# Performance work log

Hardware: AMD Instinct MI355X
Metric: run time of the kernel (lower is better)

## Reference

```python
import jax, jax.numpy as jnp
import numpy as np
from jax import lax

B = 16384
NWIRES = 4


def _conv(x, w, b):
    # NCHW conv, stride 1, SAME padding (pad 1 for k=3)
    y = lax.conv_general_dilated(x, w, (1, 1), ((1, 1), (1, 1)),
                                 dimension_numbers=("NCHW", "OIHW", "NCHW"))
    return y + b[None, :, None, None]


def _pool2(x):
    b, c, h, w = x.shape
    return x.reshape(b, c, h // 2, 2, w // 2, 2).max(axis=(3, 5))


def _apply_1q(state, U, wire):
    # state: (B,2,2,2,2) complex; U: (B,2,2) complex
    s = jnp.moveaxis(state, wire + 1, -1)
    s = jnp.einsum("bij,b...j->b...i", U, s)
    return jnp.moveaxis(s, -1, wire + 1)


def _apply_cnot(state, c, t):
    s0 = jnp.take(state, 0, axis=c + 1)
    s1 = jnp.take(state, 1, axis=c + 1)
    ta = t + 1 if t < c else t  # target axis index after removing control axis
    s1 = jnp.flip(s1, axis=ta)
    return jnp.stack([s0, s1], axis=c + 1)


def _ry(th):
    c = jnp.cos(th / 2)
    s = jnp.sin(th / 2)
    U = jnp.stack([jnp.stack([c, -s], -1), jnp.stack([s, c], -1)], -2)
    return U.astype(jnp.complex64)


def _rz(th):
    e = jnp.exp(-0.5j * th.astype(jnp.complex64))
    z = jnp.zeros_like(e)
    return jnp.stack([jnp.stack([e, z], -1), jnp.stack([z, jnp.conj(e)], -1)], -2)


def _rx(th):
    c = jnp.cos(th / 2).astype(jnp.complex64)
    s = jnp.sin(th / 2).astype(jnp.complex64)
    return jnp.stack([jnp.stack([c, -1j * s], -1), jnp.stack([-1j * s, c], -1)], -2)


def _circuit(params):
    # params: (B, 16) -> PauliZ expvals (B, 4)
    b = params.shape[0]
    state = jnp.zeros((b, 16), jnp.complex64).at[:, 0].set(1.0).reshape(b, 2, 2, 2, 2)
    for i in range(NWIRES):
        state = _apply_1q(state, _ry(params[:, 4 * i + 0]), i)
        state = _apply_1q(state, _rz(params[:, 4 * i + 1]), i)
        state = _apply_1q(state, _rx(params[:, 4 * i + 2]), i)
        state = _apply_cnot(state, i, (i + 1) % NWIRES)
    probs = state.real ** 2 + state.imag ** 2  # (B,2,2,2,2)
    zs = []
    for i in range(NWIRES):
        p = probs.sum(axis=tuple(a for a in range(1, 5) if a != i + 1))  # (B,2)
        zs.append(p[:, 0] - p[:, 1])
    return jnp.stack(zs, axis=-1)


def setup_inputs() -> dict:
    key = jax.random.key(0)
    ks = jax.random.split(key, 12)
    d = {}
    d["x"] = jax.random.normal(ks[0], (B, 1, 28, 28), jnp.float32)
    d["conv1_w"] = jax.random.normal(ks[1], (4, 1, 3, 3), jnp.float32) * 0.3
    d["conv1_b"] = jax.random.normal(ks[2], (4,), jnp.float32) * 0.1
    d["conv2_w"] = jax.random.normal(ks[3], (4, 4, 3, 3), jnp.float32) * 0.15
    d["conv2_b"] = jax.random.normal(ks[4], (4,), jnp.float32) * 0.1
    d["pl_w"] = jax.random.normal(ks[5], (16, 196), jnp.float32) * 0.07
    d["pl_b"] = jax.random.normal(ks[6], (16,), jnp.float32) * 0.05
    d["ro_w"] = jax.random.normal(ks[7], (4, 4), jnp.float32) * 0.5
    d["ro_b"] = jax.random.normal(ks[8], (4,), jnp.float32) * 0.1
    d["bn_w"] = jnp.ones((4,), jnp.float32)
    d["bn_b"] = jnp.zeros((4,), jnp.float32)
    return d


def reference(x, conv1_w, conv1_b, conv2_w, conv2_b, pl_w, pl_b, ro_w, ro_b, bn_w, bn_b):
    h = _pool2(jax.nn.relu(_conv(x, conv1_w, conv1_b)))   # (B,4,14,14)
    h = _pool2(jax.nn.relu(_conv(h, conv2_w, conv2_b)))   # (B,4,7,7)
    flat = h.reshape(x.shape[0], -1)                      # (B,196)
    params = flat @ pl_w.T + pl_b                         # (B,16)
    z = _circuit(params)                                  # (B,4)
    out = z @ ro_w.T + ro_b                               # (B,4)
    mean = out.mean(0)
    var = out.var(0)  # biased, matches torch BN training normalization
    return (out - mean) / jnp.sqrt(var + 1e-5) * bn_w + bn_b
```

## Files before the change

### kernel.cpp

```cpp
#include <hip/hip_runtime.h>
#include <math.h>

#define BATCH 16384

typedef float v2f __attribute__((ext_vector_type(2)));

__device__ __forceinline__ v2f pk_fma(v2f a, v2f b, v2f c) {
  return __builtin_elementwise_fma(a, b, c);
}
__device__ __forceinline__ v2f pk_max(v2f a, v2f b) {
  return __builtin_elementwise_max(a, b);
}

__device__ __forceinline__ unsigned bf2(float lo, float hi) {
  unsigned a = __float_as_uint(lo);
  unsigned b = __float_as_uint(hi);
  a = (a + 0x7fffu + ((a >> 16) & 1u)) >> 16;
  b = (b + 0x7fffu + ((b >> 16) & 1u)) & 0xffff0000u;
  return a | b;
}

__global__ __launch_bounds__(256) void qnat_fused(
    const float* __restrict__ x,
    const float* __restrict__ w1,
    const float* __restrict__ b1,
    const float* __restrict__ w2,
    const float* __restrict__ b2,
    const float* __restrict__ plw,
    const float* __restrict__ plb,
    const float* __restrict__ rw,
    const float* __restrict__ rb,
    float* __restrict__ pre,
    float* __restrict__ stats)
{
  __shared__ __align__(16) float h1p[4][4 * 288 + 16];
  __shared__ __align__(16) float h2[4][4][200];
  __shared__ __align__(16) uint4 plw_tb[25 * 16];
  __shared__ float s_red[4][8];

  const int tid = threadIdx.x;
  const int w = tid >> 6;
  const int lane = tid & 63;
  const int base = (blockIdx.x * 4 + w) * 4;

  #pragma unroll
  for (int j = 0; j < 2; j++) {
    int s = tid + 256 * j;
    if (s < 400) {
      int tp = s >> 4;
      int k = s & 15;
      const float4* pr = (const float4*)(plw + k * 196);
      float4 a = pr[2 * tp];
      float4 b = (tp < 24) ? pr[2 * tp + 1] : make_float4(0.f, 0.f, 0.f, 0.f);
      plw_tb[s] = make_uint4(bf2(a.x, a.y), bf2(a.z, a.w),
                             bf2(b.x, b.y), bf2(b.z, b.w));
    }
  }

  {
    float4 z4 = make_float4(0.f, 0.f, 0.f, 0.f);
    float4* hz = (float4*)&h1p[w][0];
    #pragma unroll
    for (int t = 0; t < 5; t++) {
      int p = t * 64 + lane;
      if (p < 292) hz[p] = z4;
    }
    if (lane < 16) h2[w][lane >> 2][196 + (lane & 3)] = 0.0f;
  }
  __syncthreads();

  const int i = lane >> 2;
  const int q = lane & 3;
  const bool c1act = lane < 56;

  float4 pfa[4], pfb[4];
  float pe0[4], pe1[4];
  #pragma unroll
  for (int r = 0; r < 4; r++) {
    pfa[r] = make_float4(0,0,0,0); pfb[r] = make_float4(0,0,0,0);
    pe0[r] = 0.0f; pe1[r] = 0.0f;
  }

  if (c1act) {
    const float* xb = x + (size_t)base * 784;
    #pragma unroll
    for (int r = 0; r < 4; r++) {
      int row = 2 * i - 1 + r;
      if (0 <= row && row < 28) {
        const float* rp = xb + row * 28;
        pfa[r] = *(const float4*)(rp + 8 * q);
        if (q > 0) pe0[r] = rp[8 * q - 1];
        if (q < 3) {
          pfb[r] = *(const float4*)(rp + 8 * q + 4);
          pe1[r] = rp[8 * q + 8];
        }
      }
    }
  }

  #pragma unroll 1
  for (int it = 0; it < 4; ++it) {
    if (c1act) {
      float win[4][10];
      #pragma unroll
      for (int r = 0; r < 4; r++) {
        win[r][0] = pe0[r];
        win[r][1] = pfa[r].x; win[r][2] = pfa[r].y;
        win[r][3] = pfa[r].z; win[r][4] = pfa[r].w;
        win[r][5] = pfb[r].x; win[r][6] = pfb[r].y;
        win[r][7] = pfb[r].z; win[r][8] = pfb[r].w;
        win[r][9] = pe1[r];
      }
      if (it != 3) {
        const float* xn = x + (size_t)(base + it + 1) * 784;
        #pragma unroll
        for (int r = 0; r < 4; r++) {
          int row = 2 * i - 1 + r;
          pfa[r] = make_float4(0,0,0,0);
          pfb[r] = make_float4(0,0,0,0);
          pe0[r] = 0.0f; pe1[r] = 0.0f;
          if (0 <= row && row < 28) {
            const float* rp = xn + row * 28;
            pfa[r] = *(const float4*)(rp + 8 * q);
            if (q > 0) pe0[r] = rp[8 * q - 1];
            if (q < 3) {
              pfb[r] = *(const float4*)(rp + 8 * q + 4);
              pe1[r] = rp[8 * q + 8];
            }
          }
        }
      }
      v2f P[4][9];
      #pragma unroll
      for (int r = 0; r < 4; r++)
        #pragma unroll
        for (int k = 0; k < 9; k++) P[r][k] = (v2f){win[r][k], win[r][k + 1]};

      float* hb = &h1p[w][18 * (i + 1) + 1 + 4 * q];
      #pragma unroll
      for (int c = 0; c < 4; c++) {
        const float* wc = w1 + c * 9;
        const v2f bias2 = (v2f){b1[c], b1[c]};
        v2f a0[4], a1[4];
        #pragma unroll
        for (int jj = 0; jj < 4; jj++) { a0[jj] = bias2; a1[jj] = bias2; }
        #pragma unroll
        for (int dy = 0; dy < 3; dy++)
          #pragma unroll
          for (int dx = 0; dx < 3; dx++) {
            const float wv = wc[dy * 3 + dx];
            const v2f wvv = (v2f){wv, wv};
            #pragma unroll
            for (int jj = 0; jj < 4; jj++) {
              a0[jj] = pk_fma(P[dy][2 * jj + dx],     wvv, a0[jj]);
              a1[jj] = pk_fma(P[dy + 1][2 * jj + dx], wvv, a1[jj]);
            }
          }
        float m[4];
        #pragma unroll
        for (int jj = 0; jj < 4; jj++) {
          v2f mm = pk_max(a0[jj], a1[jj]);
          m[jj] = fmaxf(fmaxf(mm.x, mm.y), 0.0f);
        }
        float* p = hb + 288 * c;
        if (q < 3) {
          p[0] = m[0];
          *(float2*)(p + 1) = make_float2(m[1], m[2]);
          p[3] = m[3];
        } else {
          p[0] = m[0];
          p[1] = m[1];
        }
      }
    }

    {
      const int jq = lane & 7;
      const int i2 = lane >> 3;
      if (i2 < 7 && jq < 7) {
        v2f acc[4][2];
        #pragma unroll
        for (int co = 0; co < 4; co++) {
          const v2f bb = (v2f){b2[co], b2[co]};
          acc[co][0] = bb; acc[co][1] = bb;
        }
        #pragma unroll
        for (int ci = 0; ci < 4; ci++) {
          const float* rp = &h1p[w][288 * ci + 36 * i2 + 2 * jq];
          v2f Q[4][3];
          #pragma unroll
          for (int r = 0; r < 4; r++) {
            v2f a = *(const v2f*)(rp + 18 * r);
            v2f b = *(const v2f*)(rp + 18 * r + 2);
            Q[r][0] = a;
            Q[r][1] = (v2f){a.y, b.x};
            Q[r][2] = b;
          }
          #pragma unroll
          for (int co = 0; co < 4; co++) {
            const float* wp = w2 + (co * 4 + ci) * 9;
            #pragma unroll
            for (int dy = 0; dy < 3; dy++)
              #pragma unroll
              for (int dx = 0; dx < 3; dx++) {
                const float wv = wp[dy * 3 + dx];
                const v2f wvv = (v2f){wv, wv};
                acc[co][0] = pk_fma(Q[dy][dx],     wvv, acc[co][0]);
                acc[co][1] = pk_fma(Q[dy + 1][dx], wvv, acc[co][1]);
              }
          }
        }
        #pragma unroll
        for (int co = 0; co < 4; co++) {
          v2f mm = pk_max(acc[co][0], acc[co][1]);
          h2[w][it][49 * co + 7 * i2 + jq] = fmaxf(fmaxf(mm.x, mm.y), 0.0f);
        }
      }
    }
  }

  const int s2 = lane >> 4;
  const int k = lane & 15;

  float cv, sv;
  {
    const float4* hv4 = (const float4*)&h2[w][s2][0];
    const uint4*  wb4 = &plw_tb[k];
    v2f sacc = (v2f){0.0f, 0.0f};
    #pragma unroll
    for (int t = 0; t < 25; t++) {
      float4 h0 = hv4[2 * t];
      float4 h1 = hv4[2 * t + 1];
      uint4 wb = wb4[16 * t];
      v2f w01 = (v2f){__uint_as_float(wb.x << 16), __uint_as_float(wb.x & 0xffff0000u)};
      v2f w23 = (v2f){__uint_as_float(wb.y << 16), __uint_as_float(wb.y & 0xffff0000u)};
      v2f w45 = (v2f){__uint_as_float(wb.z << 16), __uint_as_float(wb.z & 0xffff0000u)};
      v2f w67 = (v2f){__uint_as_float(wb.w << 16), __uint_as_float(wb.w & 0xffff0000u)};
      sacc = pk_fma((v2f){h0.x, h0.y}, w01, sacc);
      sacc = pk_fma((v2f){h0.z, h0.w}, w23, sacc);
      sacc = pk_fma((v2f){h1.x, h1.y}, w45, sacc);
      sacc = pk_fma((v2f){h1.z, h1.w}, w67, sacc);
    }
    float pv = sacc.x + sacc.y + plb[k];
    __sincosf(pv * 0.5f, &sv, &cv);
  }

  {
    const int l = k;
    const int gb = lane & 48;
    float re = (l == 0) ? 1.0f : 0.0f;
    float im = 0.0f;
    #pragma unroll
    for (int qi = 0; qi < 4; qi++) {
      const int beta = 3 - qi;
      const int m = 1 << beta;
      const int b = (l >> beta) & 1;
      float c = __shfl(cv, gb + 4 * qi, 64), s = __shfl(sv, gb + 4 * qi, 64);
      float pr_ = __shfl_xor(re, m, 64), pi_ = __shfl_xor(im, m, 64);
      float sg = b ? s : -s;
      re = fmaf(c, re, sg * pr_);
      im = fmaf(c, im, sg * pi_);
      c = __shfl(cv, gb + 4 * qi + 1, 64); s = __shfl(sv, gb + 4 * qi + 1, 64);
      float sz = b ? s : -s;
      float nr = c * re - sz * im;
      float ni = c * im + sz * re;
      re = nr; im = ni;
      c = __shfl(cv, gb + 4 * qi + 2, 64); s = __shfl(sv, gb + 4 * qi + 2, 64);
      pr_ = __shfl_xor(re, m, 64); pi_ = __shfl_xor(im, m, 64);
      nr = fmaf(c, re, s * pi_);
      ni = fmaf(c, im, -s * pr_);
      re = nr; im = ni;
      const int tm = 1 << (3 - ((qi + 1) & 3));
      float fr = __shfl_xor(re, tm, 64), fi = __shfl_xor(im, tm, 64);
      if (b) { re = fr; im = fi; }
    }
    float pr2 = re * re + im * im;
    float z0 = ((l >> 3) & 1) ? -pr2 : pr2;
    float z1 = ((l >> 2) & 1) ? -pr2 : pr2;
    float z2 = ((l >> 1) & 1) ? -pr2 : pr2;
    float z3 = (l & 1) ? -pr2 : pr2;
    #pragma unroll
    for (int off = 8; off >= 1; off >>= 1) {
      z0 += __shfl_xor(z0, off, 64);
      z1 += __shfl_xor(z1, off, 64);
      z2 += __shfl_xor(z2, off, 64);
      z3 += __shfl_xor(z3, off, 64);
    }
    float as0 = 0.f, as1 = 0.f, as2 = 0.f, as3 = 0.f;
    float aq0 = 0.f, aq1 = 0.f, aq2 = 0.f, aq3 = 0.f;
    if (l == 0) {
      float o0 = fmaf(rw[0],  z0, fmaf(rw[1],  z1, fmaf(rw[2],  z2, fmaf(rw[3],  z3, rb[0]))));
      float o1 = fmaf(rw[4],  z0, fmaf(rw[5],  z1, fmaf(rw[6],  z2, fmaf(rw[7],  z3, rb[1]))));
      float o2 = fmaf(rw[8],  z0, fmaf(rw[9],  z1, fmaf(rw[10], z2, fmaf(rw[11], z3, rb[2]))));
      float o3 = fmaf(rw[12], z0, fmaf(rw[13], z1, fmaf(rw[14], z2, fmaf(rw[15], z3, rb[3]))));
      *(float4*)(pre + (size_t)(base + s2) * 4) = make_float4(o0, o1, o2, o3);
      as0 = o0; aq0 = o0 * o0;
      as1 = o1; aq1 = o1 * o1;
      as2 = o2; aq2 = o2 * o2;
      as3 = o3; aq3 = o3 * o3;
    }
    #pragma unroll
    for (int off = 32; off >= 16; off >>= 1) {
      as0 += __shfl_down(as0, off, 64); aq0 += __shfl_down(aq0, off, 64);
      as1 += __shfl_down(as1, off, 64); aq1 += __shfl_down(aq1, off, 64);
      as2 += __shfl_down(as2, off, 64); aq2 += __shfl_down(aq2, off, 64);
      as3 += __shfl_down(as3, off, 64); aq3 += __shfl_down(aq3, off, 64);
    }
    if (lane == 0) {
      s_red[w][0] = as0; s_red[w][4] = aq0;
      s_red[w][1] = as1; s_red[w][5] = aq1;
      s_red[w][2] = as2; s_red[w][6] = aq2;
      s_red[w][3] = as3; s_red[w][7] = aq3;
    }
  }
  __syncthreads();
  if (tid < 8) {
    float v = s_red[0][tid] + s_red[1][tid] + s_red[2][tid] + s_red[3][tid];
    atomicAdd(&stats[tid], v);
  }
}

__global__ __launch_bounds__(256) void qnat_bn(
    float* __restrict__ pre,
    const float* __restrict__ stats,
    const float* __restrict__ bnw,
    const float* __restrict__ bnb)
{
  int idx = blockIdx.x * 256 + threadIdx.x;
  int c = idx & 3;
  float mean = stats[c] * (1.0f / BATCH);
  float ex2 = stats[4 + c] * (1.0f / BATCH);
  float var = ex2 - mean * mean;
  float inv = rsqrtf(var + 1e-5f);
  pre[idx] = (pre[idx] - mean) * inv * bnw[c] + bnb[c];
}

extern "C" void kernel_launch(void* const* d_in, const int* in_sizes, int n_in,
                              void* d_out, int out_size, void* d_ws, size_t ws_size,
                              hipStream_t stream) {
  const float* x   = (const float*)d_in[0];
  const float* w1  = (const float*)d_in[1];
  const float* b1  = (const float*)d_in[2];
  const float* w2  = (const float*)d_in[3];
  const float* b2  = (const float*)d_in[4];
  const float* plw = (const float*)d_in[5];
  const float* plb = (const float*)d_in[6];
  const float* rw  = (const float*)d_in[7];
  const float* rb  = (const float*)d_in[8];
  const float* bnw = (const float*)d_in[9];
  const float* bnb = (const float*)d_in[10];

  float* out   = (float*)d_out;
  float* stats = (float*)d_ws;

  hipMemsetAsync(stats, 0, 8 * sizeof(float), stream);
  qnat_fused<<<BATCH / 16, 256, 0, stream>>>(x, w1, b1, w2, b2, plw, plb, rw, rb, out, stats);
  qnat_bn<<<(BATCH * 4) / 256, 256, 0, stream>>>(out, stats, bnw, bnb);
}
```

Baseline: 133.2 us.

## Compute the 196-to-16 projection with bf16 MFMA across the block's samples

Pooled conv2 activations are stored as bf16 in a shared per-block matrix of 16 samples, not as per-wave fp32 arrays. The 196x16 linear projection now runs as seven 16x16x32 bf16 MFMA steps, replacing per-lane packed-FMA dot products, and the results are redistributed with shuffles. This needs an extra block-wide barrier because the matrix spans all waves. It also rounds the activations to bf16 and pads the weight table to 28 tiles.

```diff
diff --git a/kernel.cpp b/kernel.cpp
--- a/kernel.cpp
+++ b/kernel.cpp
@@ -4,6 +4,9 @@
 #define BATCH 16384
 
 typedef float v2f __attribute__((ext_vector_type(2)));
+typedef unsigned short u16;
+typedef __attribute__((ext_vector_type(8))) short short8;
+typedef __attribute__((ext_vector_type(4))) float f32x4;
 
 __device__ __forceinline__ v2f pk_fma(v2f a, v2f b, v2f c) {
   return __builtin_elementwise_fma(a, b, c);
@@ -18,6 +21,12 @@
   a = (a + 0x7fffu + ((a >> 16) & 1u)) >> 16;
   b = (b + 0x7fffu + ((b >> 16) & 1u)) & 0xffff0000u;
   return a | b;
+}
+
+__device__ __forceinline__ unsigned cvtpk(float lo, float hi) {
+  unsigned r;
+  asm("v_cvt_pk_bf16_f32 %0, %1, %2" : "=v"(r) : "v"(lo), "v"(hi));
+  return r;
 }
 
 __global__ __launch_bounds__(256) void qnat_fused(
@@ -34,8 +43,8 @@
     float* __restrict__ stats)
 {
   __shared__ __align__(16) float h1p[4][4 * 288 + 16];
-  __shared__ __align__(16) float h2[4][4][200];
-  __shared__ __align__(16) uint4 plw_tb[25 * 16];
+  __shared__ __align__(16) u16 h2b[16][232];
+  __shared__ __align__(16) uint4 plw_tb[28 * 16];
   __shared__ float s_red[4][8];
 
   const int tid = threadIdx.x;
@@ -46,14 +55,18 @@
   #pragma unroll
   for (int j = 0; j < 2; j++) {
     int s = tid + 256 * j;
-    if (s < 400) {
+    if (s < 448) {
       int tp = s >> 4;
-      int k = s & 15;
-      const float4* pr = (const float4*)(plw + k * 196);
-      float4 a = pr[2 * tp];
-      float4 b = (tp < 24) ? pr[2 * tp + 1] : make_float4(0.f, 0.f, 0.f, 0.f);
-      plw_tb[s] = make_uint4(bf2(a.x, a.y), bf2(a.z, a.w),
-                             bf2(b.x, b.y), bf2(b.z, b.w));
+      int k2 = s & 15;
+      uint4 v = make_uint4(0u, 0u, 0u, 0u);
+      if (tp < 25) {
+        const float4* pr = (const float4*)(plw + k2 * 196);
+        float4 a = pr[2 * tp];
+        float4 b = (tp < 24) ? pr[2 * tp + 1] : make_float4(0.f, 0.f, 0.f, 0.f);
+        v = make_uint4(bf2(a.x, a.y), bf2(a.z, a.w),
+                       bf2(b.x, b.y), bf2(b.z, b.w));
+      }
+      plw_tb[s] = v;
     }
   }
 
@@ -65,7 +78,13 @@
       int p = t * 64 + lane;
       if (p < 292) hz[p] = z4;
     }
-    if (lane < 16) h2[w][lane >> 2][196 + (lane & 3)] = 0.0f;
+    uint4 z4u = make_uint4(0u, 0u, 0u, 0u);
+    uint4* hz2 = (uint4*)h2b;
+    #pragma unroll
+    for (int t = 0; t < 2; t++) {
+      int p = tid + 256 * t;
+      if (p < 464) hz2[p] = z4u;
+    }
   }
   __syncthreads();
 
@@ -210,38 +229,47 @@
               }
           }
         }
+        float mo[4];
         #pragma unroll
         for (int co = 0; co < 4; co++) {
           v2f mm = pk_max(acc[co][0], acc[co][1]);
-          h2[w][it][49 * co + 7 * i2 + jq] = fmaxf(fmaxf(mm.x, mm.y), 0.0f);
-        }
-      }
-    }
-  }
+          mo[co] = fmaxf(fmaxf(mm.x, mm.y), 0.0f);
+        }
+        unsigned u01 = cvtpk(mo[0], mo[1]);
+        unsigned u23 = cvtpk(mo[2], mo[3]);
+        u16* hp = &h2b[w * 4 + it][7 * i2 + jq];
+        hp[0]   = (u16)u01;
+        hp[49]  = (u16)(u01 >> 16);
+        hp[98]  = (u16)u23;
+        hp[147] = (u16)(u23 >> 16);
+      }
+    }
+  }
+  __syncthreads();
 
   const int s2 = lane >> 4;
   const int k = lane & 15;
 
   float cv, sv;
   {
-    const float4* hv4 = (const float4*)&h2[w][s2][0];
-    const uint4*  wb4 = &plw_tb[k];
-    v2f sacc = (v2f){0.0f, 0.0f};
-    #pragma unroll
-    for (int t = 0; t < 25; t++) {
-      float4 h0 = hv4[2 * t];
-      float4 h1 = hv4[2 * t + 1];
-      uint4 wb = wb4[16 * t];
-      v2f w01 = (v2f){__uint_as_float(wb.x << 16), __uint_as_float(wb.x & 0xffff0000u)};
-      v2f w23 = (v2f){__uint_as_float(wb.y << 16), __uint_as_float(wb.y & 0xffff0000u)};
-      v2f w45 = (v2f){__uint_as_float(wb.z << 16), __uint_as_float(wb.z & 0xffff0000u)};
-      v2f w67 = (v2f){__uint_as_float(wb.w << 16), __uint_as_float(wb.w & 0xffff0000u)};
-      sacc = pk_fma((v2f){h0.x, h0.y}, w01, sacc);
-      sacc = pk_fma((v2f){h0.z, h0.w}, w23, sacc);
-      sacc = pk_fma((v2f){h1.x, h1.y}, w45, sacc);
-      sacc = pk_fma((v2f){h1.z, h1.w}, w67, sacc);
-    }
-    float pv = sacc.x + sacc.y + plb[k];
+    const int arow = lane & 15;
+    const int kg = lane >> 4;
+    const short8* ha = (const short8*)&h2b[arow][0];
+    const short8* hbw = (const short8*)plw_tb;
+    f32x4 acc = {0.f, 0.f, 0.f, 0.f};
+    #pragma unroll
+    for (int kt = 0; kt < 7; kt++) {
+      short8 av = ha[4 * kt + kg];
+      short8 bv = hbw[(4 * kt + kg) * 16 + arow];
+      acc = __builtin_amdgcn_mfma_f32_16x16x32_bf16(av, bv, acc, 0, 0, 0);
+    }
+    const int srcl = 16 * w + k;
+    float c0 = __shfl(acc[0], srcl, 64);
+    float c1 = __shfl(acc[1], srcl, 64);
+    float c2 = __shfl(acc[2], srcl, 64);
+    float c3 = __shfl(acc[3], srcl, 64);
+    float pv = (s2 & 2) ? ((s2 & 1) ? c3 : c2) : ((s2 & 1) ? c1 : c0);
+    pv += plb[k];
     __sincosf(pv * 0.5f, &sv, &cv);
   }
 
```

Measured after the change: 132.6 us. Within noise of the previous version (-0.5%).
